# Performance work log

Measured on AMD Instinct MI355X. Metric: run time of the kernel, lower is better.

Reference implementation:

```python
import jax, jax.numpy as jnp
import numpy as np

TEACHER_TEMP = 0.07
STUDENT_TEMP = 0.1
N_SK_ITERS = 3
SK_EPS = 1e-8
KOLEO_EPS = 1e-8


def l2norm(x, eps=1e-12):
    # matches F.normalize(p=2, dim=-1): x / max(||x||, eps)
    n = jnp.linalg.norm(x, axis=-1, keepdims=True)
    return x / jnp.maximum(n, eps)


def sinkhorn_knopp(logits, temp):
    # logits: [M, K] -> doubly-stochastic-ish Q: [M, K]
    M = logits / temp
    M = M - jnp.max(M)
    Q = jnp.exp(M).T  # [K, M]
    for _ in range(N_SK_ITERS):
        Q = Q / (jnp.sum(Q, axis=1, keepdims=True) + SK_EPS)  # normalize over samples
        Q = Q / (jnp.sum(Q, axis=0, keepdims=True) + SK_EPS)  # normalize over prototypes
    return Q.T


def koleo_loss(x):
    # DINOv2 KoLeo: -mean(log(distance to nearest neighbor))
    x = l2norm(x, KOLEO_EPS)
    n = x.shape[0]
    dots = x @ x.T  # [K, K]
    dots = jnp.where(jnp.eye(n, dtype=bool), -1.0, dots)  # exclude self (fill diag with -1)
    nn_idx = jnp.argmax(dots, axis=1)
    d = jnp.linalg.norm(x - x[nn_idx], axis=-1)
    return -jnp.mean(jnp.log(d + KOLEO_EPS))


def setup_inputs() -> dict:
    key = jax.random.key(0)
    k1, k2, k3, k4 = jax.random.split(key, 4)
    B, N, D, K = 8, 1024, 768, 8192
    return {
        "teacher_patch_tokens": jax.random.normal(k1, (B, N, D), jnp.float32),
        "student_patch_tokens": jax.random.normal(k2, (B, N, D), jnp.float32),
        "token_masks": jax.random.randint(k3, (B, N), 0, 2) > 0,
        "proto_weight": jax.random.normal(k4, (K, D), jnp.float32) * 0.02,
    }


def reference(teacher_patch_tokens, student_patch_tokens, token_masks, proto_weight):
    B, N, D = teacher_patch_tokens.shape
    K = proto_weight.shape[0]

    t = l2norm(teacher_patch_tokens)  # [B,N,D]
    s = l2norm(student_patch_tokens)

    # prototype bank = bias-free linear: logits = x @ W^T
    t_logits = jnp.einsum('bnd,kd->bnk', t, proto_weight)  # [B,N,K]

    # Sinkhorn-Knopp targets (no grad)
    Q = jax.lax.stop_gradient(
        sinkhorn_knopp(t_logits.reshape(B * N, K), TEACHER_TEMP)
    ).reshape(B, N, K)

    t_logp = jax.nn.log_softmax(t_logits / TEACHER_TEMP, axis=-1)
    teacher_proto_loss = -jnp.sum(Q * t_logp) / (B * N)

    koleo = koleo_loss(l2norm(proto_weight))

    # Student cross-entropy on masked tokens. Dense-masked formulation:
    # computes the same mean over masked positions as boolean indexing.
    s_logits = jnp.einsum('bnd,kd->bnk', s, proto_weight)
    s_logp = jax.nn.log_softmax(s_logits / STUDENT_TEMP, axis=-1)
    per_token = -jnp.sum(Q * s_logp, axis=-1)  # [B,N]
    m = token_masks.astype(per_token.dtype)
    clustering_loss = jnp.sum(per_token * m) / jnp.maximum(jnp.sum(m), 1.0)

    return jnp.stack([clustering_loss, teacher_proto_loss, koleo])
```

## Files before the change

### kernel.cpp

```cpp
#include <hip/hip_runtime.h>
#include <stdint.h>

typedef unsigned short u16;
typedef __bf16 bf16x8 __attribute__((ext_vector_type(8)));
typedef float f32x4 __attribute__((ext_vector_type(4)));
typedef unsigned short u16x8 __attribute__((ext_vector_type(8)));
typedef unsigned short u16x4 __attribute__((ext_vector_type(4)));

#define SK_EPS 1e-8f
#define S_T 20.60992915555662f
#define S_S 14.426950408889634f
#define INV_TT 14.285714285714286f
#define INV_TS 10.0f

__device__ __forceinline__ float b2f(u16 u){ return __uint_as_float(((unsigned)u)<<16); }
__device__ __forceinline__ u16 f2b(float f){
  unsigned u = __float_as_uint(f);
  u += 0x7FFFu + ((u>>16)&1u);
  return (u16)(u>>16);
}
__device__ __forceinline__ unsigned encf(float x){ unsigned u=__float_as_uint(x); return (u&0x80000000u)? ~u : (u|0x80000000u); }
__device__ __forceinline__ float decf(unsigned u){ return (u&0x80000000u)? __uint_as_float(u&0x7FFFFFFFu) : __uint_as_float(~u); }

__device__ __forceinline__ void gload16(const void* g, void* l){
  __builtin_amdgcn_global_load_lds((const __attribute__((address_space(1))) void*)g,
                                   (__attribute__((address_space(3))) void*)l, 16, 0, 0);
}

__global__ __launch_bounds__(192) void norm_cast(const float* __restrict__ in, u16* __restrict__ out,
                                                 u16* __restrict__ out2, int donorm){
  int row = blockIdx.x, tid = threadIdx.x;
  const float4* p = (const float4*)(in + (size_t)row*768);
  float4 v = p[tid];
  float ss = v.x*v.x + v.y*v.y + v.z*v.z + v.w*v.w;
  #pragma unroll
  for (int off=1; off<64; off<<=1) ss += __shfl_xor(ss, off);
  __shared__ float smem[3];
  int wv = tid>>6;
  if ((tid&63)==0) smem[wv] = ss;
  __syncthreads();
  float tot = smem[0]+smem[1]+smem[2];
  float scale = donorm ? (1.0f/fmaxf(sqrtf(tot), 1e-12f)) : 1.0f;
  u16x4 o;
  o[0]=f2b(v.x); o[1]=f2b(v.y); o[2]=f2b(v.z); o[3]=f2b(v.w);
  u16x4 on;
  on[0]=f2b(v.x*scale); on[1]=f2b(v.y*scale); on[2]=f2b(v.z*scale); on[3]=f2b(v.w*scale);
  if (out2){
    *(u16x4*)(out  + (size_t)row*768 + tid*4) = o;
    *(u16x4*)(out2 + (size_t)row*768 + tid*4) = on;
  } else {
    *(u16x4*)(out + (size_t)row*768 + tid*4) = donorm ? on : o;
  }
}

template<int MODE>
__global__ __launch_bounds__(256) void gemm_bt(
    const u16* __restrict__ A, const u16* __restrict__ B, int Ndim, int Kd,
    u16* __restrict__ Cout, float* __restrict__ colC,
    const u16* __restrict__ Tl, const float* __restrict__ a3, const float* __restrict__ b3,
    float* __restrict__ sexp, float* __restrict__ sdot, unsigned* __restrict__ maxd)
{
  __shared__ __align__(16) u16 As[128*64];
  __shared__ __align__(16) u16 Bs[128*64];
  int tid = threadIdx.x, lane = tid & 63, wave = tid >> 6;
  int wr = wave >> 1, wc = wave & 1;

  int bid = blockIdx.x, tm, tn;
  if (gridDim.x == 4096){
    int xcd = bid & 7, local = bid >> 3;
    int g = local >> 6, w = local & 63;
    tm = xcd*8 + (w >> 3);
    tn = g*8 + (w & 7);
  } else { int nbn = Ndim >> 7; tm = bid / nbn; tn = bid % nbn; }
  int m0 = tm<<7, n0 = tn<<7;

  const f32x4 fzero = {0.f,0.f,0.f,0.f};
  f32x4 acc[4][4];
  #pragma unroll
  for (int i=0;i<4;++i)
    #pragma unroll
    for (int j=0;j<4;++j) acc[i][j] = fzero;

  int srcRow = lane>>3;
  int srcCol = (((lane&7) ^ (lane>>3)) << 3);

  int nkt = Kd>>6;
  for (int kt=0; kt<nkt; ++kt){
    if (kt) __syncthreads();
    int k0 = kt<<6;
    #pragma unroll
    for (int c=0;c<4;++c){
      int chunk = (wave<<2)+c;
      int row = (chunk<<3) + srcRow;
      gload16(A + (size_t)(m0+row)*Kd + k0 + srcCol, (void*)(As + (chunk<<9)));
      gload16(B + (size_t)(n0+row)*Kd + k0 + srcCol, (void*)(Bs + (chunk<<9)));
    }
    asm volatile("s_waitcnt vmcnt(0)" ::: "memory");
    __syncthreads();
    #pragma unroll
    for (int ks=0; ks<2; ++ks){
      bf16x8 af[4], bfr[4];
      #pragma unroll
      for (int f=0; f<4; ++f){
        int rowA = (wr<<6)+(f<<4)+(lane&15);
        int idxA = ((rowA<<6) + (ks<<5) + ((lane>>4)<<3)) ^ ((lane&7)<<3);
        af[f] = *(const bf16x8*)(const void*)(As + idxA);
        int rowB = (wc<<6)+(f<<4)+(lane&15);
        int idxB = ((rowB<<6) + (ks<<5) + ((lane>>4)<<3)) ^ ((lane&7)<<3);
        bfr[f] = *(const bf16x8*)(const void*)(Bs + idxB);
      }
      #pragma unroll
      for (int fm=0;fm<4;++fm)
        #pragma unroll
        for (int fn=0;fn<4;++fn)
          acc[fm][fn] = __builtin_amdgcn_mfma_f32_16x16x32_bf16(af[fm], bfr[fn], acc[fm][fn], 0,0,0);
    }
  }

  if constexpr (MODE == 0){
    float cs[4] = {0.f,0.f,0.f,0.f};
    #pragma unroll
    for (int fm=0;fm<4;++fm)
      #pragma unroll
      for (int j=0;j<4;++j){
        size_t gr = (size_t)(m0 + (wr<<6)+(fm<<4)+((lane>>4)<<2)+j);
        #pragma unroll
        for (int fn=0;fn<4;++fn){
          int cl = (wc<<6)+(fn<<4)+(lane&15);
          u16 hb = f2b(acc[fm][fn][j]);
          Cout[gr*(size_t)Ndim + n0+cl] = hb;
          cs[fn] += exp2f(b2f(hb)*S_T);
        }
      }
    #pragma unroll
    for (int fn=0;fn<4;++fn){
      float v = cs[fn];
      v += __shfl_xor(v,16); v += __shfl_xor(v,32);
      if (lane < 16) atomicAdd(&colC[n0 + (wc<<6)+(fn<<4)+lane], v);
    }
  } else if constexpr (MODE == 1){
    #pragma unroll
    for (int fm=0;fm<4;++fm)
      #pragma unroll
      for (int j=0;j<4;++j){
        size_t gr = (size_t)(m0 + (wr<<6)+(fm<<4)+((lane>>4)<<2)+j);
        float sx=0.f, sd=0.f;
        #pragma unroll
        for (int fn=0;fn<4;++fn){
          int cl = (wc<<6)+(fn<<4)+(lane&15);
          size_t gc = (size_t)(n0+cl);
          float v = acc[fm][fn][j];
          float tl = b2f(Tl[gr*(size_t)Ndim + gc]);
          sx += exp2f(v*S_S);
          sd += exp2f(tl*S_T)*a3[gc]*v;
        }
        #pragma unroll
        for (int off=1; off<16; off<<=1){ sx += __shfl_xor(sx,off); sd += __shfl_xor(sd,off); }
        if ((lane&15)==0){
          atomicAdd(&sexp[gr], sx);
          atomicAdd(&sdot[gr], b3[gr]*sd);
        }
      }
  } else {
    #pragma unroll
    for (int fm=0;fm<4;++fm)
      #pragma unroll
      for (int j=0;j<4;++j){
        size_t gr = (size_t)(m0 + (wr<<6)+(fm<<4)+((lane>>4)<<2)+j);
        float mx = -2.0f;
        #pragma unroll
        for (int fn=0;fn<4;++fn){
          int cl = (wc<<6)+(fn<<4)+(lane&15);
          size_t gc = (size_t)(n0+cl);
          float v = acc[fm][fn][j];
          if (gr != gc) mx = fmaxf(mx, v);
        }
        #pragma unroll
        for (int off=1; off<16; off<<=1) mx = fmaxf(mx, __shfl_xor(mx,off));
        if ((lane&15)==0) atomicMax(&maxd[gr], encf(mx));
      }
  }
}

__global__ __launch_bounds__(256) void sk_colsum(const u16* __restrict__ L, const float* __restrict__ bvec,
                                                 float* __restrict__ colOut, int Kc, int useb){
  int tid = threadIdx.x;
  int c0 = blockIdx.x*2048 + tid*8;
  int r0 = blockIdx.y*64;
  float acc[8] = {0.f,0.f,0.f,0.f,0.f,0.f,0.f,0.f};
  for (int r=r0; r<r0+64; ++r){
    u16x8 v = *(const u16x8*)(L + (size_t)r*Kc + c0);
    float bm = useb ? bvec[r] : 1.0f;
    #pragma unroll
    for (int i=0;i<8;++i) acc[i] += exp2f(b2f(v[i])*S_T)*bm;
  }
  #pragma unroll
  for (int i=0;i<8;++i) atomicAdd(&colOut[c0+i], acc[i]);
}

__global__ __launch_bounds__(256) void sk_rowsum(const u16* __restrict__ L, const float* __restrict__ avec,
    float* __restrict__ rowR, float* __restrict__ rowRE, float* __restrict__ rowT, int Kc, int mode){
  int m = blockIdx.x, tid = threadIdx.x;
  const u16* Lr = L + (size_t)m*Kc;
  float sR=0.f, sRE=0.f, sT=0.f;
  int nit = Kc/2048;
  for (int it=0; it<nit; ++it){
    int c = it*2048 + tid*8;
    u16x8 v = *(const u16x8*)(Lr + c);
    f32x4 alo = *(const f32x4*)(avec+c);
    f32x4 ahi = *(const f32x4*)(avec+c+4);
    #pragma unroll
    for (int i=0;i<8;++i){
      float l = b2f(v[i]);
      float E = exp2f(l*S_T);
      float a = (i<4)? alo[i] : ahi[i-4];
      float Ea = E*a;
      sR += Ea;
      if (mode&1) sRE += E;
      if (mode&2) sT += Ea*l;
    }
  }
  #pragma unroll
  for (int off=1; off<64; off<<=1){
    sR += __shfl_xor(sR,off);
    sRE += __shfl_xor(sRE,off);
    sT += __shfl_xor(sT,off);
  }
  __shared__ float red[3][4];
  int wv = tid>>6;
  if ((tid&63)==0){ red[0][wv]=sR; red[1][wv]=sRE; red[2][wv]=sT; }
  __syncthreads();
  if (tid==0){
    rowR[m] = red[0][0]+red[0][1]+red[0][2]+red[0][3];
    if (mode&1) rowRE[m] = red[1][0]+red[1][1]+red[1][2]+red[1][3];
    if (mode&2) rowT[m]  = red[2][0]+red[2][1]+red[2][2]+red[2][3];
  }
}

__global__ void upd_col(float* aV, float* colC, int K, int first){
  int k = blockIdx.x*256+threadIdx.x;
  if (k<K){
    float s = colC[k];
    float p = first ? 1.0f : aV[k];
    aV[k] = p/(p*s + SK_EPS);
    colC[k] = 0.0f;
  }
}
__global__ void upd_row(float* bV, const float* rowR, int M, int first){
  int m = blockIdx.x*256+threadIdx.x;
  if (m<M){
    float R = rowR[m];
    float p = first ? 1.0f : bV[m];
    bV[m] = p/(p*R + SK_EPS);
  }
}
__global__ void fin_rows(float* bV, const float* rowR, const float* rowRE, const float* rowT,
                         float* sumQ, float* ttok, int M){
  int m = blockIdx.x*256+threadIdx.x;
  if (m<M){
    float p = bV[m], R = rowR[m];
    float b3 = p/(p*R + SK_EPS);
    bV[m] = b3;
    float sq = b3*R;
    sumQ[m] = sq;
    ttok[m] = logf(rowRE[m])*sq - b3*rowT[m]*INV_TT;
  }
}

__global__ __launch_bounds__(1024) void finalize(const unsigned char* __restrict__ mask,
    const float* __restrict__ sexp, const float* __restrict__ sdot,
    const float* __restrict__ sumQ, const float* __restrict__ ttok,
    const unsigned* __restrict__ maxd, float* __restrict__ out, int M, int K){
  int tid = threadIdx.x;
  __shared__ int isBool;
  if (tid==0) isBool = 0;
  __syncthreads();
  int f = 0;
  for (int i=tid; i<M; i+=1024) if ((i&3) && mask[i]) f = 1;
  if (f) isBool = 1;
  __syncthreads();
  int ib = isBool;
  float cn=0.f, cc=0.f, ts=0.f, ks=0.f;
  for (int m=tid; m<M; m+=1024){
    int mk = ib ? (mask[m]!=0) : (((const int*)mask)[m]!=0);
    float pt = logf(sexp[m])*sumQ[m] - sdot[m]*INV_TS;
    if (mk){ cn += pt; cc += 1.0f; }
    ts += ttok[m];
  }
  for (int k=tid; k<K; k+=1024){
    float d = decf(maxd[k]);
    ks += logf(sqrtf(fmaxf(2.0f-2.0f*d, 0.0f)) + SK_EPS);
  }
  #pragma unroll
  for (int off=1; off<64; off<<=1){
    cn += __shfl_xor(cn,off); cc += __shfl_xor(cc,off);
    ts += __shfl_xor(ts,off); ks += __shfl_xor(ks,off);
  }
  __shared__ float red[4][16];
  int wv = tid>>6;
  if ((tid&63)==0){ red[0][wv]=cn; red[1][wv]=cc; red[2][wv]=ts; red[3][wv]=ks; }
  __syncthreads();
  if (tid==0){
    float CN=0,CC=0,TS=0,KS=0;
    for (int i=0;i<16;++i){ CN+=red[0][i]; CC+=red[1][i]; TS+=red[2][i]; KS+=red[3][i]; }
    out[0] = CN/fmaxf(CC,1.0f);
    out[1] = TS/(float)M;
    out[2] = -KS/(float)K;
  }
}

extern "C" void kernel_launch(void* const* d_in, const int* in_sizes, int n_in,
                              void* d_out, int out_size, void* d_ws, size_t ws_size,
                              hipStream_t stream){
  const float* teacher = (const float*)d_in[0];
  const float* student = (const float*)d_in[1];
  const unsigned char* mask = (const unsigned char*)d_in[2];
  const float* proto = (const float*)d_in[3];
  const int D = 768;
  const int M = in_sizes[0]/D;
  const int K = in_sizes[3]/D;
  float* out = (float*)d_out;

  char* ws = (char*)d_ws;
  size_t off = 0;
  auto alloc = [&](size_t bytes)->void*{ void* p = ws+off; off += (bytes+255)&~(size_t)255; return p; };
  u16* t_logits = (u16*)alloc((size_t)M*K*2);
  u16* t_hat    = (u16*)alloc((size_t)M*D*2);
  u16* s_hat    = (u16*)alloc((size_t)M*D*2);
  u16* w_bf     = (u16*)alloc((size_t)K*D*2);
  u16* w_hat    = (u16*)alloc((size_t)K*D*2);
  float* colC   = (float*)alloc((size_t)K*4);
  float* sexp   = (float*)alloc((size_t)M*4);
  float* sdot   = (float*)alloc((size_t)M*4);
  unsigned* maxd= (unsigned*)alloc((size_t)K*4);
  float* aV     = (float*)alloc((size_t)K*4);
  float* bV     = (float*)alloc((size_t)M*4);
  float* rowR   = (float*)alloc((size_t)M*4);
  float* rowRE  = (float*)alloc((size_t)M*4);
  float* rowT   = (float*)alloc((size_t)M*4);
  float* sumQ   = (float*)alloc((size_t)M*4);
  float* ttok   = (float*)alloc((size_t)M*4);

  hipMemsetAsync(colC, 0, (size_t)K*4, stream);
  hipMemsetAsync(sexp, 0, (size_t)M*4, stream);
  hipMemsetAsync(sdot, 0, (size_t)M*4, stream);
  hipMemsetAsync(maxd, 0, (size_t)K*4, stream);

  norm_cast<<<M, 192, 0, stream>>>(teacher, t_hat, nullptr, 1);
  norm_cast<<<M, 192, 0, stream>>>(student, s_hat, nullptr, 1);
  norm_cast<<<K, 192, 0, stream>>>(proto, w_bf, w_hat, 1);

  int nblk = (M/128)*(K/128);
  gemm_bt<0><<<nblk, 256, 0, stream>>>(t_hat, w_bf, K, D, t_logits, colC,
                                       nullptr,nullptr,nullptr,nullptr,nullptr,nullptr);

  dim3 cgrid(K/2048, M/64);
  upd_col<<<(K+255)/256, 256, 0, stream>>>(aV, colC, K, 1);
  sk_rowsum<<<M, 256, 0, stream>>>(t_logits, aV, rowR, rowRE, rowT, K, 1);
  upd_row<<<(M+255)/256, 256, 0, stream>>>(bV, rowR, M, 1);
  sk_colsum<<<cgrid, 256, 0, stream>>>(t_logits, bV, colC, K, 1);
  upd_col<<<(K+255)/256, 256, 0, stream>>>(aV, colC, K, 0);
  sk_rowsum<<<M, 256, 0, stream>>>(t_logits, aV, rowR, rowRE, rowT, K, 0);
  upd_row<<<(M+255)/256, 256, 0, stream>>>(bV, rowR, M, 0);
  sk_colsum<<<cgrid, 256, 0, stream>>>(t_logits, bV, colC, K, 1);
  upd_col<<<(K+255)/256, 256, 0, stream>>>(aV, colC, K, 0);
  sk_rowsum<<<M, 256, 0, stream>>>(t_logits, aV, rowR, rowRE, rowT, K, 2);
  fin_rows<<<(M+255)/256, 256, 0, stream>>>(bV, rowR, rowRE, rowT, sumQ, ttok, M);

  gemm_bt<1><<<nblk, 256, 0, stream>>>(s_hat, w_bf, K, D, nullptr, nullptr,
                                       t_logits, aV, bV, sexp, sdot, nullptr);
  gemm_bt<2><<<nblk, 256, 0, stream>>>(w_hat, w_hat, K, D, nullptr, nullptr,
                                       nullptr,nullptr,nullptr,nullptr,nullptr, maxd);

  finalize<<<1, 1024, 0, stream>>>(mask, sexp, sdot, sumQ, ttok, maxd, out, M, K);
}
```

Baseline: 733.5 us.

## Fuse teacher and student GEMMs sharing prototype tiles; exploit symmetry in KoLeo GEMM

Adds a dual-mode GEMM that computes the teacher and student logits together, so each prototype tile loaded into shared memory is reused for both. Student logits are written out as bf16 and their cross-entropy dot term is folded into the last Sinkhorn row-sum pass, which removes the separate student GEMM. The KoLeo Gram GEMM now computes only upper-triangle tiles and applies each off-diagonal tile to both row and column maxima, roughly halving that work. In exchange the fused GEMM uses more registers and LDS, and writing and rereading a 64M-entry bf16 student logits buffer adds memory traffic. The fused path only runs when the workspace is large enough to hold that buffer.

```diff
diff --git a/kernel.cpp b/kernel.cpp
--- a/kernel.cpp
+++ b/kernel.cpp
@@ -55,23 +55,33 @@
 
 template<int MODE>
 __global__ __launch_bounds__(256) void gemm_bt(
-    const u16* __restrict__ A, const u16* __restrict__ B, int Ndim, int Kd,
-    u16* __restrict__ Cout, float* __restrict__ colC,
+    const u16* __restrict__ A, const u16* __restrict__ A2, const u16* __restrict__ B,
+    int Ndim, int Kd,
+    u16* __restrict__ Cout, u16* __restrict__ Cout2,
+    float* __restrict__ colC, float* __restrict__ sexp,
     const u16* __restrict__ Tl, const float* __restrict__ a3, const float* __restrict__ b3,
-    float* __restrict__ sexp, float* __restrict__ sdot, unsigned* __restrict__ maxd)
+    float* __restrict__ sdot, unsigned* __restrict__ maxd)
 {
-  __shared__ __align__(16) u16 As[128*64];
-  __shared__ __align__(16) u16 Bs[128*64];
+  __shared__ __align__(16) u16 As[8192];
+  __shared__ __align__(16) u16 Bs[8192];
+  __shared__ __align__(16) u16 As2[(MODE==3)?8192:16];
   int tid = threadIdx.x, lane = tid & 63, wave = tid >> 6;
   int wr = wave >> 1, wc = wave & 1;
 
   int bid = blockIdx.x, tm, tn;
-  if (gridDim.x == 4096){
+  if constexpr (MODE == 2){
     int xcd = bid & 7, local = bid >> 3;
-    int g = local >> 6, w = local & 63;
-    tm = xcd*8 + (w >> 3);
-    tn = g*8 + (w & 7);
-  } else { int nbn = Ndim >> 7; tm = bid / nbn; tn = bid % nbn; }
+    tm = xcd + ((local >> 6) << 3);
+    tn = local & 63;
+    if (tn < tm) return;
+  } else {
+    if (gridDim.x == 4096){
+      int xcd = bid & 7, local = bid >> 3;
+      int g = local >> 6, w = local & 63;
+      tm = xcd*8 + (w >> 3);
+      tn = g*8 + (w & 7);
+    } else { int nbn = Ndim >> 7; tm = bid / nbn; tn = bid % nbn; }
+  }
   int m0 = tm<<7, n0 = tn<<7;
 
   const f32x4 fzero = {0.f,0.f,0.f,0.f};
@@ -80,6 +90,13 @@
   for (int i=0;i<4;++i)
     #pragma unroll
     for (int j=0;j<4;++j) acc[i][j] = fzero;
+  f32x4 acc2[(MODE==3)?4:1][4];
+  if constexpr (MODE==3){
+    #pragma unroll
+    for (int i=0;i<4;++i)
+      #pragma unroll
+      for (int j=0;j<4;++j) acc2[i][j] = fzero;
+  }
 
   int srcRow = lane>>3;
   int srcCol = (((lane&7) ^ (lane>>3)) << 3);
@@ -93,6 +110,8 @@
       int chunk = (wave<<2)+c;
       int row = (chunk<<3) + srcRow;
       gload16(A + (size_t)(m0+row)*Kd + k0 + srcCol, (void*)(As + (chunk<<9)));
+      if constexpr (MODE==3)
+        gload16(A2 + (size_t)(m0+row)*Kd + k0 + srcCol, (void*)(As2 + (chunk<<9)));
       gload16(B + (size_t)(n0+row)*Kd + k0 + srcCol, (void*)(Bs + (chunk<<9)));
     }
     asm volatile("s_waitcnt vmcnt(0)" ::: "memory");
@@ -102,34 +121,61 @@
       bf16x8 af[4], bfr[4];
       #pragma unroll
       for (int f=0; f<4; ++f){
+        int rowB = (wc<<6)+(f<<4)+(lane&15);
+        int idxB = ((rowB<<6) + (ks<<5) + ((lane>>4)<<3)) ^ ((lane&7)<<3);
+        bfr[f] = *(const bf16x8*)(const void*)(Bs + idxB);
+      }
+      #pragma unroll
+      for (int f=0; f<4; ++f){
         int rowA = (wr<<6)+(f<<4)+(lane&15);
         int idxA = ((rowA<<6) + (ks<<5) + ((lane>>4)<<3)) ^ ((lane&7)<<3);
         af[f] = *(const bf16x8*)(const void*)(As + idxA);
-        int rowB = (wc<<6)+(f<<4)+(lane&15);
-        int idxB = ((rowB<<6) + (ks<<5) + ((lane>>4)<<3)) ^ ((lane&7)<<3);
-        bfr[f] = *(const bf16x8*)(const void*)(Bs + idxB);
       }
       #pragma unroll
       for (int fm=0;fm<4;++fm)
         #pragma unroll
         for (int fn=0;fn<4;++fn)
           acc[fm][fn] = __builtin_amdgcn_mfma_f32_16x16x32_bf16(af[fm], bfr[fn], acc[fm][fn], 0,0,0);
+      if constexpr (MODE==3){
+        #pragma unroll
+        for (int f=0; f<4; ++f){
+          int rowA = (wr<<6)+(f<<4)+(lane&15);
+          int idxA = ((rowA<<6) + (ks<<5) + ((lane>>4)<<3)) ^ ((lane&7)<<3);
+          af[f] = *(const bf16x8*)(const void*)(As2 + idxA);
+        }
+        #pragma unroll
+        for (int fm=0;fm<4;++fm)
+          #pragma unroll
+          for (int fn=0;fn<4;++fn)
+            acc2[fm][fn] = __builtin_amdgcn_mfma_f32_16x16x32_bf16(af[fm], bfr[fn], acc2[fm][fn], 0,0,0);
+      }
     }
   }
 
-  if constexpr (MODE == 0){
+  if constexpr (MODE == 0 || MODE == 3){
     float cs[4] = {0.f,0.f,0.f,0.f};
     #pragma unroll
     for (int fm=0;fm<4;++fm)
       #pragma unroll
       for (int j=0;j<4;++j){
         size_t gr = (size_t)(m0 + (wr<<6)+(fm<<4)+((lane>>4)<<2)+j);
+        float sx = 0.f;
         #pragma unroll
         for (int fn=0;fn<4;++fn){
           int cl = (wc<<6)+(fn<<4)+(lane&15);
           u16 hb = f2b(acc[fm][fn][j]);
           Cout[gr*(size_t)Ndim + n0+cl] = hb;
           cs[fn] += exp2f(b2f(hb)*S_T);
+          if constexpr (MODE==3){
+            u16 hs = f2b(acc2[fm][fn][j]);
+            Cout2[gr*(size_t)Ndim + n0+cl] = hs;
+            sx += exp2f(b2f(hs)*S_S);
+          }
+        }
+        if constexpr (MODE==3){
+          #pragma unroll
+          for (int off=1; off<16; off<<=1) sx += __shfl_xor(sx,off);
+          if ((lane&15)==0) atomicAdd(&sexp[gr], sx);
         }
       }
     #pragma unroll
@@ -161,7 +207,7 @@
           atomicAdd(&sdot[gr], b3[gr]*sd);
         }
       }
-  } else {
+  } else if constexpr (MODE == 2){
     #pragma unroll
     for (int fm=0;fm<4;++fm)
       #pragma unroll
@@ -179,6 +225,19 @@
         for (int off=1; off<16; off<<=1) mx = fmaxf(mx, __shfl_xor(mx,off));
         if ((lane&15)==0) atomicMax(&maxd[gr], encf(mx));
       }
+    if (tm != tn){
+      #pragma unroll
+      for (int fn=0;fn<4;++fn){
+        float mx = -2.0f;
+        #pragma unroll
+        for (int fm=0;fm<4;++fm)
+          #pragma unroll
+          for (int j=0;j<4;++j) mx = fmaxf(mx, acc[fm][fn][j]);
+        mx = fmaxf(mx, __shfl_xor(mx,16));
+        mx = fmaxf(mx, __shfl_xor(mx,32));
+        if (lane < 16) atomicMax(&maxd[n0 + (wc<<6)+(fn<<4)+lane], encf(mx));
+      }
+    }
   }
 }
 
@@ -198,15 +257,20 @@
   for (int i=0;i<8;++i) atomicAdd(&colOut[c0+i], acc[i]);
 }
 
-__global__ __launch_bounds__(256) void sk_rowsum(const u16* __restrict__ L, const float* __restrict__ avec,
-    float* __restrict__ rowR, float* __restrict__ rowRE, float* __restrict__ rowT, int Kc, int mode){
+__global__ __launch_bounds__(256) void sk_rowsum(const u16* __restrict__ L, const u16* __restrict__ S,
+    const float* __restrict__ avec,
+    float* __restrict__ rowR, float* __restrict__ rowRE, float* __restrict__ rowT,
+    float* __restrict__ rowS, int Kc, int mode){
   int m = blockIdx.x, tid = threadIdx.x;
   const u16* Lr = L + (size_t)m*Kc;
-  float sR=0.f, sRE=0.f, sT=0.f;
+  const u16* Sr = (mode&4) ? (S + (size_t)m*Kc) : nullptr;
+  float sR=0.f, sRE=0.f, sT=0.f, sS=0.f;
   int nit = Kc/2048;
   for (int it=0; it<nit; ++it){
     int c = it*2048 + tid*8;
     u16x8 v = *(const u16x8*)(Lr + c);
+    u16x8 sv;
+    if (mode&4) sv = *(const u16x8*)(Sr + c);
     f32x4 alo = *(const f32x4*)(avec+c);
     f32x4 ahi = *(const f32x4*)(avec+c+4);
     #pragma unroll
@@ -218,6 +282,7 @@
       sR += Ea;
       if (mode&1) sRE += E;
       if (mode&2) sT += Ea*l;
+      if (mode&4) sS += Ea*b2f(sv[i]);
     }
   }
   #pragma unroll
@@ -225,15 +290,17 @@
     sR += __shfl_xor(sR,off);
     sRE += __shfl_xor(sRE,off);
     sT += __shfl_xor(sT,off);
-  }
-  __shared__ float red[3][4];
+    sS += __shfl_xor(sS,off);
+  }
+  __shared__ float red[4][4];
   int wv = tid>>6;
-  if ((tid&63)==0){ red[0][wv]=sR; red[1][wv]=sRE; red[2][wv]=sT; }
+  if ((tid&63)==0){ red[0][wv]=sR; red[1][wv]=sRE; red[2][wv]=sT; red[3][wv]=sS; }
   __syncthreads();
   if (tid==0){
     rowR[m] = red[0][0]+red[0][1]+red[0][2]+red[0][3];
     if (mode&1) rowRE[m] = red[1][0]+red[1][1]+red[1][2]+red[1][3];
     if (mode&2) rowT[m]  = red[2][0]+red[2][1]+red[2][2]+red[2][3];
+    if (mode&4) rowS[m]  = red[3][0]+red[3][1]+red[3][2]+red[3][3];
   }
 }
 
@@ -255,7 +322,8 @@
   }
 }
 __global__ void fin_rows(float* bV, const float* rowR, const float* rowRE, const float* rowT,
-                         float* sumQ, float* ttok, int M){
+                         const float* rowS, const float* sexp,
+                         float* sumQ, float* ttok, float* ptok, int M, int havePt){
   int m = blockIdx.x*256+threadIdx.x;
   if (m<M){
     float p = bV[m], R = rowR[m];
@@ -264,13 +332,15 @@
     float sq = b3*R;
     sumQ[m] = sq;
     ttok[m] = logf(rowRE[m])*sq - b3*rowT[m]*INV_TT;
+    if (havePt) ptok[m] = logf(sexp[m])*sq - b3*rowS[m]*INV_TS;
   }
 }
 
 __global__ __launch_bounds__(1024) void finalize(const unsigned char* __restrict__ mask,
+    const float* __restrict__ ptok,
     const float* __restrict__ sexp, const float* __restrict__ sdot,
     const float* __restrict__ sumQ, const float* __restrict__ ttok,
-    const unsigned* __restrict__ maxd, float* __restrict__ out, int M, int K){
+    const unsigned* __restrict__ maxd, float* __restrict__ out, int M, int K, int usePt){
   int tid = threadIdx.x;
   __shared__ int isBool;
   if (tid==0) isBool = 0;
@@ -283,7 +353,7 @@
   float cn=0.f, cc=0.f, ts=0.f, ks=0.f;
   for (int m=tid; m<M; m+=1024){
     int mk = ib ? (mask[m]!=0) : (((const int*)mask)[m]!=0);
-    float pt = logf(sexp[m])*sumQ[m] - sdot[m]*INV_TS;
+    float pt = usePt ? ptok[m] : (logf(sexp[m])*sumQ[m] - sdot[m]*INV_TS);
     if (mk){ cn += pt; cc += 1.0f; }
     ts += ttok[m];
   }
@@ -338,8 +408,12 @@
   float* rowR   = (float*)alloc((size_t)M*4);
   float* rowRE  = (float*)alloc((size_t)M*4);
   float* rowT   = (float*)alloc((size_t)M*4);
+  float* rowS   = (float*)alloc((size_t)M*4);
   float* sumQ   = (float*)alloc((size_t)M*4);
   float* ttok   = (float*)alloc((size_t)M*4);
+  float* ptok   = (float*)alloc((size_t)M*4);
+  u16* s_logits = (u16*)alloc((size_t)M*K*2);
+  int dual = (off <= ws_size);
 
   hipMemsetAsync(colC, 0, (size_t)K*4, stream);
   hipMemsetAsync(sexp, 0, (size_t)M*4, stream);
@@ -351,26 +425,34 @@
   norm_cast<<<K, 192, 0, stream>>>(proto, w_bf, w_hat, 1);
 
   int nblk = (M/128)*(K/128);
-  gemm_bt<0><<<nblk, 256, 0, stream>>>(t_hat, w_bf, K, D, t_logits, colC,
-                                       nullptr,nullptr,nullptr,nullptr,nullptr,nullptr);
+  if (dual){
+    gemm_bt<3><<<nblk, 256, 0, stream>>>(t_hat, s_hat, w_bf, K, D, t_logits, s_logits,
+                                         colC, sexp, nullptr, nullptr, nullptr, nullptr, nullptr);
+  } else {
+    gemm_bt<0><<<nblk, 256, 0, stream>>>(t_hat, nullptr, w_bf, K, D, t_logits, nullptr,
+                                         colC, nullptr, nullptr, nullptr, nullptr, nullptr, nullptr);
+  }
 
   dim3 cgrid(K/2048, M/64);
   upd_col<<<(K+255)/256, 256, 0, stream>>>(aV, colC, K, 1);
-  sk_rowsum<<<M, 256, 0, stream>>>(t_logits, aV, rowR, rowRE, rowT, K, 1);
+  sk_rowsum<<<M, 256, 0, stream>>>(t_logits, nullptr, aV, rowR, rowRE, rowT, rowS, K, 1);
   upd_row<<<(M+255)/256, 256, 0, stream>>>(bV, rowR, M, 1);
   sk_colsum<<<cgrid, 256, 0, stream>>>(t_logits, bV, colC, K, 1);
   upd_col<<<(K+255)/256, 256, 0, stream>>>(aV, colC, K, 0);
-  sk_rowsum<<<M, 256, 0, stream>>>(t_logits, aV, rowR, rowRE, rowT, K, 0);
+  sk_rowsum<<<M, 256, 0, stream>>>(t_logits, nullptr, aV, rowR, rowRE, rowT, rowS, K, 0);
   upd_row<<<(M+255)/256, 256, 0, stream>>>(bV, rowR, M, 0);
   sk_colsum<<<cgrid, 256, 0, stream>>>(t_logits, bV, colC, K, 1);
   upd_col<<<(K+255)/256, 256, 0, stream>>>(aV, colC, K, 0);
-  sk_rowsum<<<M, 256, 0, stream>>>(t_logits, aV, rowR, rowRE, rowT, K, 2);
-  fin_rows<<<(M+255)/256, 256, 0, stream>>>(bV, rowR, rowRE, rowT, sumQ, ttok, M);
-
-  gemm_bt<1><<<nblk, 256, 0, stream>>>(s_hat, w_bf, K, D, nullptr, nullptr,
-                                       t_logits, aV, bV, sexp, sdot, nullptr);
-  gemm_bt<2><<<nblk, 256, 0, stream>>>(w_hat, w_hat, K, D, nullptr, nullptr,
-                                       nullptr,nullptr,nullptr,nullptr,nullptr, maxd);
-
-  finalize<<<1, 1024, 0, stream>>>(mask, sexp, sdot, sumQ, ttok, maxd, out, M, K);
-}
+  sk_rowsum<<<M, 256, 0, stream>>>(t_logits, s_logits, aV, rowR, rowRE, rowT, rowS, K, dual ? 6 : 2);
+  fin_rows<<<(M+255)/256, 256, 0, stream>>>(bV, rowR, rowRE, rowT, rowS, sexp,
+                                            sumQ, ttok, ptok, M, dual);
+
+  if (!dual){
+    gemm_bt<1><<<nblk, 256, 0, stream>>>(s_hat, nullptr, w_bf, K, D, nullptr, nullptr,
+                                         nullptr, sexp, t_logits, aV, bV, sdot, nullptr);
+  }
+  gemm_bt<2><<<nblk, 256, 0, stream>>>(w_hat, nullptr, w_hat, K, D, nullptr, nullptr,
+                                       nullptr, nullptr, nullptr, nullptr, nullptr, nullptr, maxd);
+
+  finalize<<<1, 1024, 0, stream>>>(mask, ptok, sexp, sdot, sumQ, ttok, maxd, out, M, K, dual);
+}
```

Result: slower. 757.4 us (+3.2%).
